# Optimization experiments

Hardware: AMD Instinct MI355X
Metric: run time of the kernel (lower is better)

## Reference

```python
import jax, jax.numpy as jnp
import numpy as np


def _pairwise_sq(x, y):
    # squared euclidean distances [B,N,M] via gram trick (avoids [B,N,M,D] temp)
    x2 = jnp.sum(x * x, -1)[:, :, None]
    y2 = jnp.sum(y * y, -1)[:, None, :]
    return x2 + y2 - 2.0 * jnp.einsum('bnd,bmd->bnm', x, y)


def _dtw_dp(C):
    # Subsequence DTW accumulated-cost matrix. C: [N,M].
    # D[0,:] = C[0,:] (free start anywhere in y);
    # D[i,j] = C[i,j] + min(D[i-1,j], D[i-1,j-1], D[i,j-1]).
    # Within-row recurrence D[i,j] = min(a[j], D[i,j-1] + C[i,j]) with
    # a[j] = min(D[i-1,j], D[i-1,j-1]) + C[i,j] is a min-plus prefix scan:
    # D[i,j] = S[j] + cummin(a - S)[j], S = cumsum(C[i]).
    inf = jnp.asarray(jnp.inf, C.dtype)
    def row(Dprev, Crow):
        shifted = jnp.concatenate([jnp.full((1,), inf, C.dtype), Dprev[:-1]])
        a = jnp.minimum(Dprev, shifted) + Crow
        S = jnp.cumsum(Crow)
        D = S + jax.lax.cummin(a - S)
        return D, D
    _, Dr = jax.lax.scan(row, C[0], C[1:])
    return jnp.concatenate([C[0][None], Dr], 0)


def _backtrack(D):
    # Backtrack optimal subseq-DTW path from (N-1, argmin D[-1]) to row 0.
    # Returns, per x index i, the largest y index aligned to i on the path
    # (== last occurrence kept by dict(dtw_path) in the torch code).
    N, M = D.shape
    inf = jnp.asarray(jnp.inf, D.dtype)
    j0 = jnp.argmin(D[-1]).astype(jnp.int32)
    i0 = jnp.asarray(N - 1, jnp.int32)
    yl = jnp.zeros((N,), jnp.int32).at[i0].set(j0)
    def step(carry, _):
        i, j, yl = carry
        dd = jnp.where(j > 0, D[i - 1, j - 1], inf)
        du = D[i - 1, j]
        dl = jnp.where(j > 0, D[i, j - 1], inf)
        best = jnp.minimum(jnp.minimum(dd, du), dl)
        take_d = dd == best
        take_u = (~take_d) & (du == best)
        ni = jnp.where(take_d | take_u, i - 1, i)
        nj = jnp.where(take_d, j - 1, jnp.where(take_u, j, j - 1))
        active = i > 0
        ni = jnp.where(active, ni, i)
        nj = jnp.where(active, nj, j)
        yl = jnp.where(active, yl.at[ni].max(nj), yl)
        return (ni, nj, yl), None
    (_, _, yl), _ = jax.lax.scan(step, (i0, j0, yl), None, length=N + M)
    return yl


def setup_inputs() -> dict:
    key = jax.random.key(0)
    k0, k1, k2, k3 = jax.random.split(key, 4)
    B, N, M, D = 16, 1024, 4096, 64
    return {
        'x': jax.random.normal(k0, (B, N, D), jnp.float32),
        'y': jax.random.normal(k1, (B, M, D), jnp.float32),
        'x_t': jax.random.uniform(k2, (B, N), dtype=jnp.float32),
        'y_t': jax.random.uniform(k3, (B, M), dtype=jnp.float32),
    }


def reference(x, y, x_t, y_t):
    C = _pairwise_sq(x, y)                      # [B,N,M]
    D = jax.vmap(_dtw_dp)(C)                    # [B,N,M]
    # total path cost == DP optimum (sum of C along the optimal path)
    dtw_cost = jnp.min(D[:, -1, :], axis=-1)    # [B]
    y_last = jax.vmap(_backtrack)(jax.lax.stop_gradient(D))  # [B,N] int32
    w_ts = x_t                                  # path covers all x indices 0..N-1 in order
    w_vs = jnp.take_along_axis(y_t, y_last, axis=1)
    return dtw_cost, w_ts, w_vs
```

## Files before the change

### kernel.cpp

```cpp
#include <hip/hip_runtime.h>

#define B_ 16
#define N_ 1024
#define M_ 4096
#define D_ 64
#define SROWS_ (N_ + 63)
#define SROWSP_ (SROWS_ + 17)
#define SPAIR_ 544
#define TSB_ ((size_t)SPAIR_ * 128)
#define BTQ_ 96
#define BTROWS_ 128
#define GEMM_BLKS_ 2048

__device__ __forceinline__ float finf() { return __builtin_inff(); }

__device__ __forceinline__ float wave_shr1(float x) {
  return __int_as_float(__builtin_amdgcn_update_dpp(
      0, __float_as_int(x), 0x138, 0xF, 0xF, false));
}
__device__ __forceinline__ float rdlane(float v, int l) {
  return __int_as_float(__builtin_amdgcn_readlane(__float_as_int(v), l));
}

__global__ void prep_kernel(const float* __restrict__ x,
                            const float* __restrict__ x_t,
                            float* __restrict__ x2,
                            float* __restrict__ w_ts_out) {
  int id = blockIdx.x * blockDim.x + threadIdx.x;
  const float4* xr = (const float4*)(x + (size_t)id * D_);
  float s = 0.f;
#pragma unroll
  for (int e = 0; e < D_ / 4; ++e) {
    float4 v = xr[e];
    s += v.x * v.x + v.y * v.y + v.z * v.z + v.w * v.w;
  }
  x2[id] = s;
  w_ts_out[id] = x_t[id];
}

__device__ __forceinline__ void gemm_body(
    const float* __restrict__ x, const float* __restrict__ y,
    const float* __restrict__ x2, float* __restrict__ Cs, int chunkBase,
    int b, int tile, int ibeg, int t, char* smem) {
  float4* ylds = (float4*)smem;
  float4* xlds = (float4*)(smem + 65536);
  float* y2lds = (float*)(smem + 73728);
  const int cg = t & 63;
  const int rg = t >> 6;
  float* CsT = Cs + (size_t)(b * 4 + tile) * SROWSP_ * 256;

  {
    const int j = chunkBase + tile * 256 + t;
    const float4* yrow = (const float4*)(y + ((size_t)b * M_ + j) * D_);
    float4 yr[16];
#pragma unroll
    for (int e = 0; e < 16; ++e) yr[e] = yrow[e];
    float y2 = 0.f;
#pragma unroll
    for (int e = 0; e < 16; ++e)
      y2 += yr[e].x * yr[e].x + yr[e].y * yr[e].y + yr[e].z * yr[e].z +
            yr[e].w * yr[e].w;
    y2lds[t] = y2;
#pragma unroll
    for (int e = 0; e < 16; ++e) ylds[e * 256 + t] = yr[e];
  }
  if (t < 128) {
    const int row = t >> 2;
    const int part = t & 3;
    const float4* xr = (const float4*)(x + ((size_t)b * N_ + ibeg + row) * D_);
#pragma unroll
    for (int k = 0; k < 4; ++k) {
      const int e = part * 4 + k;
      xlds[e * 32 + row] = xr[e];
    }
  }
  __syncthreads();

  const int r0 = rg * 8;
  float acc[8][4];
#pragma unroll
  for (int r = 0; r < 8; ++r)
#pragma unroll
    for (int c = 0; c < 4; ++c) acc[r][c] = 0.f;

#pragma unroll
  for (int kb = 0; kb < 4; ++kb) {
    float4 yf[4][4];
#pragma unroll
    for (int c = 0; c < 4; ++c)
#pragma unroll
      for (int ee = 0; ee < 4; ++ee)
        yf[c][ee] = ylds[(kb * 4 + ee) * 256 + cg + 64 * c];
#pragma unroll
    for (int r = 0; r < 8; ++r) {
      float4 xv[4];
#pragma unroll
      for (int ee = 0; ee < 4; ++ee)
        xv[ee] = xlds[(kb * 4 + ee) * 32 + r0 + r];
#pragma unroll
      for (int ee = 0; ee < 4; ++ee) {
#pragma unroll
        for (int c = 0; c < 4; ++c) {
          acc[r][c] += xv[ee].x * yf[c][ee].x + xv[ee].y * yf[c][ee].y +
                       xv[ee].z * yf[c][ee].z + xv[ee].w * yf[c][ee].w;
        }
      }
    }
  }

#pragma unroll
  for (int r = 0; r < 8; ++r) {
    const int i = ibeg + r0 + r;
    const float xx = x2[b * N_ + i];
#pragma unroll
    for (int c = 0; c < 4; ++c) {
      const int ct = cg + 64 * c;
      const int l = ct >> 2;
      CsT[(size_t)(i + l) * 256 + ct] = xx + y2lds[ct] - 2.f * acc[r][c];
    }
  }
}

__global__ __launch_bounds__(256) void gemm_kernel(
    const float* __restrict__ x, const float* __restrict__ y,
    const float* __restrict__ x2, float* __restrict__ Cs, int chunkBase) {
  __shared__ __align__(16) char smem[74752];
  gemm_body(x, y, x2, Cs, chunkBase, blockIdx.z, blockIdx.x, blockIdx.y * 32,
            threadIdx.x, smem);
}

__global__ __launch_bounds__(256) void dtw_fused(
    const float* __restrict__ x, const float* __restrict__ y,
    const float* __restrict__ x2, const float* __restrict__ CsRead,
    float* __restrict__ CsWrite, int nextBase,
    unsigned char* __restrict__ dec, const float* __restrict__ carryIn,
    float* __restrict__ carryOut, float* __restrict__ partV,
    int* __restrict__ partJ, int chunk, int hasCarry) {
  __shared__ __align__(16) char smem[90112];
  const int bid = blockIdx.x;
  const int t = threadIdx.x;

  if (bid >= B_) {
    const int gb = bid - B_;
    gemm_body(x, y, x2, CsWrite, nextBase, gb >> 7, gb & 3,
              ((gb >> 2) & 31) * 32, t, smem);
    return;
  }

  float(*ring)[1024] = reinterpret_cast<float(*)[1024]>(smem);
  float* cring = reinterpret_cast<float*>(smem + 12288);
  int* prog = reinterpret_cast<int*>(smem + 16384);
  float* redV = reinterpret_cast<float*>(smem + 16400);
  int* redJ = reinterpret_cast<int*>(smem + 16416);
  volatile int* vProg = prog;

  const int b = bid;
  const int lane = t & 63;
  const int W = t >> 6;

  if (t < 3) prog[t] = -1;
  const float* cIn = carryIn + b * N_;
  if (hasCarry) ((float4*)cring)[t] = ((const float4*)cIn)[t];
  __syncthreads();

  const float INF = finf();
  const float* loadP = CsRead + (size_t)(b * 4 + W) * SROWSP_ * 256;
  const int tileG = chunk * 4 + W;
  unsigned short* decP =
      (unsigned short*)(dec + (size_t)(b * 16 + tileG) * TSB_) + lane;
  float* carryB = carryOut + b * N_;
  const int jbase = tileG * 256 + lane * 4;

  float4 cc0 = ((const float4*)(loadP + 0 * 256))[lane];
  float4 cc1 = ((const float4*)(loadP + 1 * 256))[lane];
  float4 cc2 = ((const float4*)(loadP + 2 * 256))[lane];
  float4 cc3 = ((const float4*)(loadP + 3 * 256))[lane];
  float4 cc4 = ((const float4*)(loadP + 4 * 256))[lane];
  float4 cc5 = ((const float4*)(loadP + 5 * 256))[lane];
  float4 cc6 = ((const float4*)(loadP + 6 * 256))[lane];
  float4 cc7 = ((const float4*)(loadP + 7 * 256))[lane];
  loadP += 8 * 256;

  float edgeVec = INF, lvPrev = INF;
  float up0 = 0.f, up1 = 0.f, up2 = 0.f, up3 = 0.f;
  float dpp1 = INF, dpp2 = INF;
  float fin0 = INF, fin1 = INF, fin2 = INF, fin3 = INF;
  float ebuf[8];

#define BLOCKHEAD()                                                           \
  {                                                                           \
    if (W > 0) {                                                              \
      if (sb < N_) {                                                          \
        const int tgt = sb + 7;                                               \
        while (vProg[W - 1] < tgt) {}                                         \
        asm volatile("" ::: "memory");                                        \
        lvPrev = rdlane(edgeVec, 7);                                          \
        edgeVec = ring[W - 1][(sb + lane) & 1023];                            \
      }                                                                       \
    } else if (hasCarry) {                                                    \
      lvPrev = rdlane(edgeVec, 7);                                            \
      if (sb < N_) edgeVec = cring[(sb + lane) & 1023];                       \
    }                                                                         \
  }

#define DPSTEP(KK, CCV, ROW0, FIN)                                            \
  {                                                                           \
    const float lv = rdlane(edgeVec, (KK));                                   \
    const float left = (lane == 0) ? lv : dpp1;                               \
    const float diag = (lane == 0) ? lvPrev : dpp2;                           \
    lvPrev = lv;                                                              \
    float bv0 = fminf(diag, fminf(up0, left));                                \
    unsigned int pk = (diag <= bv0) ? 0u : ((up0 <= bv0) ? 1u : 2u);          \
    if (ROW0) bv0 = (sb + (KK) == lane) ? 0.f : bv0;                          \
    const float D0 = CCV.x + bv0;                                             \
    float bv1 = fminf(up0, fminf(up1, D0));                                   \
    pk |= (up0 <= bv1) ? 0u : ((up1 <= bv1) ? 4u : 8u);                       \
    if (ROW0) bv1 = (sb + (KK) == lane) ? 0.f : bv1;                          \
    const float D1 = CCV.y + bv1;                                             \
    float bv2 = fminf(up1, fminf(up2, D1));                                   \
    pk |= (up1 <= bv2) ? 0u : ((up2 <= bv2) ? 16u : 32u);                     \
    if (ROW0) bv2 = (sb + (KK) == lane) ? 0.f : bv2;                          \
    const float D2 = CCV.z + bv2;                                             \
    float bv3 = fminf(up2, fminf(up3, D2));                                   \
    pk |= (up2 <= bv3) ? 0u : ((up3 <= bv3) ? 64u : 128u);                    \
    if (ROW0) bv3 = (sb + (KK) == lane) ? 0.f : bv3;                          \
    const float D3 = CCV.w + bv3;                                             \
    ebuf[(KK)] = D3;                                                          \
    if ((KK) & 1) {                                                           \
      pk16 |= pk << 8;                                                        \
      decP[((KK) >> 1) * 64] = (unsigned short)pk16;                          \
    } else {                                                                  \
      pk16 = pk;                                                              \
    }                                                                         \
    if (FIN) {                                                                \
      const bool lr = (sb + (KK) == 1023 + lane);                             \
      fin0 = lr ? D0 : fin0; fin1 = lr ? D1 : fin1;                           \
      fin2 = lr ? D2 : fin2; fin3 = lr ? D3 : fin3;                           \
    }                                                                         \
    const float sh = wave_shr1(D3);                                           \
    dpp2 = dpp1; dpp1 = sh;                                                   \
    up0 = D0; up1 = D1; up2 = D2; up3 = D3;                                   \
    CCV = ((const float4*)(loadP + (KK) * 256))[lane];                        \
  }

#define BLOCKEND()                                                            \
  {                                                                           \
    const int r0 = sb - 63;                                                   \
    if (W < 3) {                                                              \
      if (lane == 63 && r0 > -8 && r0 < N_) {                                 \
        _Pragma("unroll") for (int k = 0; k < 8; ++k) {                       \
          const int r = r0 + k;                                               \
          if ((unsigned)r < (unsigned)N_) ring[W][r] = ebuf[k];               \
        }                                                                     \
        __builtin_amdgcn_s_waitcnt(0xC07F);                                   \
        vProg[W] = r0 + 7;                                                    \
      }                                                                       \
    } else if (chunk < 3) {                                                   \
      if (lane == 63 && r0 > -8 && r0 < N_) {                                 \
        _Pragma("unroll") for (int k = 0; k < 8; ++k) {                       \
          const int r = r0 + k;                                               \
          if ((unsigned)r < (unsigned)N_) carryB[r] = ebuf[k];                \
        }                                                                     \
      }                                                                       \
    }                                                                         \
    loadP += 8 * 256;                                                         \
    decP += 256;                                                              \
  }

#define STEP8(R0, FN)                                                         \
  DPSTEP(0, cc0, R0, FN) DPSTEP(1, cc1, R0, FN) DPSTEP(2, cc2, R0, FN)        \
  DPSTEP(3, cc3, R0, FN) DPSTEP(4, cc4, R0, FN) DPSTEP(5, cc5, R0, FN)        \
  DPSTEP(6, cc6, R0, FN) DPSTEP(7, cc7, R0, FN)

  int sb = 0;
  for (; sb < 64; sb += 8) {
    BLOCKHEAD();
    unsigned int pk16;
    STEP8(1, 0)
    BLOCKEND();
  }
  for (; sb < 1016; sb += 8) {
    BLOCKHEAD();
    unsigned int pk16;
    STEP8(0, 0)
    BLOCKEND();
  }
  for (; sb < 1088; sb += 8) {
    BLOCKHEAD();
    unsigned int pk16;
    STEP8(0, 1)
    BLOCKEND();
  }
#undef DPSTEP
#undef STEP8
#undef BLOCKHEAD
#undef BLOCKEND

  float mv = fin0; int mj = jbase;
  if (fin1 < mv) { mv = fin1; mj = jbase + 1; }
  if (fin2 < mv) { mv = fin2; mj = jbase + 2; }
  if (fin3 < mv) { mv = fin3; mj = jbase + 3; }
#pragma unroll
  for (int off = 32; off > 0; off >>= 1) {
    const float ov = __shfl_down(mv, off);
    const int oj = __shfl_down(mj, off);
    if (ov < mv || (ov == mv && oj < mj)) { mv = ov; mj = oj; }
  }
  if (lane == 0) { redV[W] = mv; redJ[W] = mj; }
  __syncthreads();
  if (t == 0) {
    float bm = redV[0]; int bj = redJ[0];
#pragma unroll
    for (int w = 1; w < 4; ++w)
      if (redV[w] < bm) { bm = redV[w]; bj = redJ[w]; }
    partV[b * 4 + chunk] = bm;
    partJ[b * 4 + chunk] = bj;
  }
}

__global__ __launch_bounds__(64) void backtrack_kernel(
    const unsigned char* __restrict__ dec, const float* __restrict__ partV,
    const int* __restrict__ partJ, int nch, const float* __restrict__ y_t,
    float* __restrict__ w_vs, float* __restrict__ cost_out) {
  const int b = blockIdx.x;
  const int lane = threadIdx.x;
  __shared__ unsigned int stage[3 * 3072];
  __shared__ unsigned short tab[BTROWS_][BTQ_ * 4 + 2];
  __shared__ int st_i, st_j;
  __shared__ int jrow[BTROWS_ + 1];
  const unsigned char* db = dec + (size_t)b * 16 * TSB_;
  const float* yt = y_t + b * M_;
  float* wv = w_vs + b * N_;

  if (lane == 0) {
    float bc = finf(); int bj = 0;
    for (int c = 0; c < nch; ++c) {
      const float v = partV[b * nch + c];
      const int j = partJ[b * nch + c];
      if (v < bc) { bc = v; bj = j; }
    }
    cost_out[b] = bc;
    st_i = N_ - 1;
    st_j = bj;
    wv[N_ - 1] = yt[bj];
  }
  for (;;) {
    __syncthreads();
    const int i = st_i, j = st_j;
    if (i <= 0) break;
    const int qj = j >> 2;
    int qlo = qj - (BTQ_ - 1);
    if (qlo < 0) qlo = 0;
    const int Tbase = qlo >> 6;
    int plo = (i - 127) >> 1;
    if (plo < 0) plo = 0;

#pragma unroll
    for (int tt = 0; tt < 3; ++tt) {
      int T = Tbase + tt;
      if (T > 15) T = 15;
      const uint4* src =
          (const uint4*)(db + (size_t)T * TSB_ + (size_t)plo * 128);
#pragma unroll
      for (int v = 0; v < 12; ++v) {
        const int wb = tt * 12288 + (v * 64 + lane) * 16;
        const int sw = wb ^ (((wb >> 7) & 7) << 4);
        *(uint4*)((char*)stage + sw) = src[v * 64 + lane];
      }
    }
    __syncthreads();

    const unsigned char* sb8 = (const unsigned char*)stage;
#pragma unroll
    for (int half = 0; half < 2; ++half) {
      const int r = i - lane - half * 64;
      if (r >= 1) {
        unsigned char wr[BTQ_];
#pragma unroll
        for (int k = 0; k < BTQ_; ++k) {
          const int q = qlo + k;
          const int tt = (q >> 6) - Tbase;
          const int l = q & 63;
          const int s = r + l;
          int idx = tt * 12288 + ((s >> 1) - plo) * 128 + l * 2 + (s & 1);
          idx ^= ((idx >> 7) & 7) << 4;
          wr[k] = sb8[idx];
        }
        unsigned short run = 0xFFFF;
        const int tr = lane + half * 64;
#pragma unroll
        for (int k = 0; k < BTQ_; ++k) {
          const unsigned int byte = wr[k];
#pragma unroll
          for (int cs = 0; cs < 4; ++cs) {
            const unsigned int code = (byte >> (2 * cs)) & 3u;
            const int c = 4 * k + cs;
            const unsigned short v =
                (code != 2u) ? (unsigned short)((c << 2) | code) : run;
            tab[tr][c] = v;
            run = v;
          }
        }
      }
    }
    __syncthreads();
    if (lane == 0) {
      const int base = qlo << 2;
      int rr = i, cj = j;
      while (rr >= 1 && (i - rr) < BTROWS_) {
        const int l = i - rr;
        const int c = cj - base;
        if (c < 0) break;
        const unsigned short v = tab[l][c];
        if (v == 0xFFFF) { cj = base - 1; break; }
        const int e = v >> 2;
        const int ce = v & 3;
        cj = base + e - (ce == 0 ? 1 : 0);
        --rr;
        jrow[i - rr] = cj;
      }
      st_i = rr;
      st_j = cj;
    }
    __syncthreads();
    const int cnt = i - st_i;
    if (lane < cnt) wv[i - 1 - lane] = yt[jrow[lane + 1]];
    {
      const int l2 = lane + 64;
      if (l2 < cnt) wv[i - 1 - l2] = yt[jrow[l2 + 1]];
    }
  }
}

extern "C" void kernel_launch(void* const* d_in, const int* in_sizes, int n_in,
                              void* d_out, int out_size, void* d_ws, size_t ws_size,
                              hipStream_t stream) {
  const float* x = (const float*)d_in[0];
  const float* y = (const float*)d_in[1];
  const float* x_t = (const float*)d_in[2];
  const float* y_t = (const float*)d_in[3];

  float* out_cost = (float*)d_out;
  float* out_wts = out_cost + B_;
  float* out_wvs = out_wts + B_ * N_;

  const size_t csBytes = (size_t)B_ * 4 * SROWSP_ * 256 * 4;
  const size_t decBytes = (size_t)B_ * 16 * TSB_;
  const size_t x2Bytes = (size_t)B_ * N_ * 4;
  const size_t tailBytes = x2Bytes + 2 * (size_t)B_ * N_ * 4 + B_ * 4 * 8;

  const int overlap = ws_size >= 2 * csBytes + decBytes + tailBytes;
  const int nCs = overlap ? 2 : 1;

  char* ws = (char*)d_ws;
  float* CsA = (float*)ws;
  float* CsB = overlap ? (float*)(ws + csBytes) : CsA;
  unsigned char* dec = (unsigned char*)(ws + (size_t)nCs * csBytes);
  float* x2 = (float*)(ws + (size_t)nCs * csBytes + decBytes);
  float* carryA = x2 + B_ * N_;
  float* carryB = carryA + B_ * N_;
  float* partV = carryB + B_ * N_;
  int* partJ = (int*)(partV + B_ * 4);

  prep_kernel<<<dim3((B_ * N_) / 256), 256, 0, stream>>>(x, x_t, x2, out_wts);

  float* cbuf[2] = {carryA, carryB};
  if (overlap) {
    gemm_kernel<<<dim3(4, N_ / 32, B_), 256, 0, stream>>>(x, y, x2, CsA, 0);
    for (int c = 0; c < 4; ++c) {
      float* csR = (c & 1) ? CsB : CsA;
      float* csW = (c & 1) ? CsA : CsB;
      const int nblk = B_ + (c < 3 ? GEMM_BLKS_ : 0);
      dtw_fused<<<dim3(nblk), 256, 0, stream>>>(
          x, y, x2, csR, csW, (c + 1) * 1024, dec, cbuf[(c + 1) & 1],
          cbuf[c & 1], partV, partJ, c, c > 0 ? 1 : 0);
    }
  } else {
    for (int c = 0; c < 4; ++c) {
      gemm_kernel<<<dim3(4, N_ / 32, B_), 256, 0, stream>>>(x, y, x2, CsA,
                                                            c * 1024);
      dtw_fused<<<dim3(B_), 256, 0, stream>>>(
          x, y, x2, CsA, CsA, 0, dec, cbuf[(c + 1) & 1], cbuf[c & 1], partV,
          partJ, c, c > 0 ? 1 : 0);
    }
  }

  backtrack_kernel<<<dim3(B_), 64, 0, stream>>>(dec, partV, partJ, 4, y_t,
                                                out_wvs, out_cost);
}
```

Measured before the change: 1.012 ms.

## Pipeline DTW column chunks across concurrent blocks with global progress flags

Adds a single persistent dtw_pipe kernel in which each batch gets four DP blocks, one per 1024-column chunk. Each block waits on a GEMM completion counter and then on a per-row carry progress flag published through global memory, so the chunks run as a wavefront instead of as four serialized launches. The GEMM blocks for later chunks run inside the same launch, and the full cost matrix is stored when workspace allows. This removes the inter-launch serialization and the one-block-per-batch DP bottleneck. In exchange it relies on spin-waiting across blocks, which can deadlock if the dependent blocks are not co-resident, and it needs a much larger workspace.

```diff
diff --git a/kernel.cpp b/kernel.cpp
--- a/kernel.cpp
+++ b/kernel.cpp
@@ -25,8 +25,11 @@
 __global__ void prep_kernel(const float* __restrict__ x,
                             const float* __restrict__ x_t,
                             float* __restrict__ x2,
-                            float* __restrict__ w_ts_out) {
+                            float* __restrict__ w_ts_out,
+                            int* __restrict__ ctrl) {
   int id = blockIdx.x * blockDim.x + threadIdx.x;
+  if (ctrl && blockIdx.x == 0 && threadIdx.x < 128)
+    ctrl[threadIdx.x] = (threadIdx.x < 64) ? 0 : -1;
   const float4* xr = (const float4*)(x + (size_t)id * D_);
   float s = 0.f;
 #pragma unroll
@@ -40,17 +43,16 @@
 
 __device__ __forceinline__ void gemm_body(
     const float* __restrict__ x, const float* __restrict__ y,
-    const float* __restrict__ x2, float* __restrict__ Cs, int chunkBase,
-    int b, int tile, int ibeg, int t, char* smem) {
+    const float* __restrict__ x2, float* __restrict__ CsT, int jcol0,
+    int b, int ibeg, int t, char* smem) {
   float4* ylds = (float4*)smem;
   float4* xlds = (float4*)(smem + 65536);
   float* y2lds = (float*)(smem + 73728);
+
   const int cg = t & 63;
   const int rg = t >> 6;
-  float* CsT = Cs + (size_t)(b * 4 + tile) * SROWSP_ * 256;
-
   {
-    const int j = chunkBase + tile * 256 + t;
+    const int j = jcol0 + t;
     const float4* yrow = (const float4*)(y + ((size_t)b * M_ + j) * D_);
     float4 yr[16];
 #pragma unroll
@@ -123,10 +125,241 @@
 
 __global__ __launch_bounds__(256) void gemm_kernel(
     const float* __restrict__ x, const float* __restrict__ y,
-    const float* __restrict__ x2, float* __restrict__ Cs, int chunkBase) {
+    const float* __restrict__ x2, float* __restrict__ Cs, int chunkBase,
+    int nt, int tileOff) {
   __shared__ __align__(16) char smem[74752];
-  gemm_body(x, y, x2, Cs, chunkBase, blockIdx.z, blockIdx.x, blockIdx.y * 32,
+  const int tile = blockIdx.x;
+  const int b = blockIdx.z;
+  float* CsT =
+      Cs + ((size_t)b * nt + tileOff + tile) * SROWSP_ * 256;
+  gemm_body(x, y, x2, CsT, chunkBase + tile * 256, b, blockIdx.y * 32,
             threadIdx.x, smem);
+}
+
+__global__ __launch_bounds__(256) void dtw_pipe(
+    const float* __restrict__ x, const float* __restrict__ y,
+    const float* __restrict__ x2, float* __restrict__ Cs,
+    unsigned char* __restrict__ dec, float* __restrict__ carryPipe,
+    int* __restrict__ gemmCnt, int* __restrict__ carryProg,
+    float* __restrict__ partV, int* __restrict__ partJ) {
+  __shared__ __align__(16) char smem[90112];
+  const int bid = blockIdx.x;
+  const int t = threadIdx.x;
+
+  if (bid >= 64) {
+    const int gb = bid - 64;
+    const int chunk = 1 + (gb >> 11);
+    const int g2 = gb & 2047;
+    const int b = g2 >> 7;
+    const int tile = g2 & 3;
+    const int ibeg = ((g2 >> 2) & 31) * 32;
+    float* CsT =
+        Cs + ((size_t)b * 16 + chunk * 4 + tile) * SROWSP_ * 256;
+    gemm_body(x, y, x2, CsT, chunk * 1024 + tile * 256, b, ibeg, t, smem);
+    __syncthreads();
+    if (t == 0) {
+      __threadfence();
+      atomicAdd(&gemmCnt[b * 4 + chunk], 1);
+    }
+    return;
+  }
+
+  const int b = bid >> 2;
+  const int C = bid & 3;
+  const int lane = t & 63;
+  const int W = t >> 6;
+
+  float(*ring)[1024] = reinterpret_cast<float(*)[1024]>(smem);
+  int* prog = reinterpret_cast<int*>(smem + 12288);
+  float* redV = reinterpret_cast<float*>(smem + 12352);
+  int* redJ = reinterpret_cast<int*>(smem + 12384);
+  volatile int* vProg = prog;
+
+  if (t < 3) prog[t] = -1;
+
+  if (C > 0) {
+    if (t == 0) {
+      while (__hip_atomic_load(&gemmCnt[b * 4 + C], __ATOMIC_ACQUIRE,
+                               __HIP_MEMORY_SCOPE_AGENT) < 128)
+        __builtin_amdgcn_s_sleep(8);
+      __threadfence();
+    }
+    __syncthreads();
+  } else {
+    __syncthreads();
+  }
+
+  const float INF = finf();
+  const float* loadP = Cs + ((size_t)b * 16 + C * 4 + W) * SROWSP_ * 256;
+  const int tileG = C * 4 + W;
+  unsigned short* decP =
+      (unsigned short*)(dec + (size_t)(b * 16 + tileG) * TSB_) + lane;
+  const float* carryIn = carryPipe + ((size_t)b * 3 + (C > 0 ? C - 1 : 0)) * N_;
+  float* carryOut = carryPipe + ((size_t)b * 3 + (C < 3 ? C : 0)) * N_;
+  int* progIn = &carryProg[b * 4 + (C > 0 ? C - 1 : 0)];
+  int* progOut = &carryProg[b * 4 + C];
+  const int jbase = tileG * 256 + lane * 4;
+
+  float4 cc0 = ((const float4*)(loadP + 0 * 256))[lane];
+  float4 cc1 = ((const float4*)(loadP + 1 * 256))[lane];
+  float4 cc2 = ((const float4*)(loadP + 2 * 256))[lane];
+  float4 cc3 = ((const float4*)(loadP + 3 * 256))[lane];
+  float4 cc4 = ((const float4*)(loadP + 4 * 256))[lane];
+  float4 cc5 = ((const float4*)(loadP + 5 * 256))[lane];
+  float4 cc6 = ((const float4*)(loadP + 6 * 256))[lane];
+  float4 cc7 = ((const float4*)(loadP + 7 * 256))[lane];
+  loadP += 8 * 256;
+
+  float edgeVec = INF, lvPrev = INF;
+  float up0 = 0.f, up1 = 0.f, up2 = 0.f, up3 = 0.f;
+  float dpp1 = INF, dpp2 = INF;
+  float fin0 = INF, fin1 = INF, fin2 = INF, fin3 = INF;
+  float ebuf[8];
+
+#define BLOCKHEADP()                                                          \
+  {                                                                           \
+    if (W > 0) {                                                              \
+      if (sb < N_) {                                                          \
+        const int tgt = sb + 7;                                               \
+        while (vProg[W - 1] < tgt) {}                                         \
+        asm volatile("" ::: "memory");                                        \
+        lvPrev = rdlane(edgeVec, 7);                                          \
+        edgeVec = ring[W - 1][(sb + lane) & 1023];                            \
+      }                                                                       \
+    } else if (C > 0) {                                                       \
+      if (((sb & 63) == 0) && sb < N_) {                                      \
+        const int tgt = sb + 63;                                              \
+        if (lane == 0) {                                                      \
+          while (__hip_atomic_load(progIn, __ATOMIC_ACQUIRE,                  \
+                                   __HIP_MEMORY_SCOPE_AGENT) < tgt)           \
+            __builtin_amdgcn_s_sleep(4);                                      \
+        }                                                                     \
+        edgeVec = carryIn[(sb + lane) & 1023];                                \
+      }                                                                       \
+    }                                                                         \
+  }
+
+#define DPSTEP(KK, CCV, ROW0, FIN)                                            \
+  {                                                                           \
+    const float lv = rdlane(edgeVec, eb + (KK));                              \
+    const float left = (lane == 0) ? lv : dpp1;                               \
+    const float diag = (lane == 0) ? lvPrev : dpp2;                           \
+    lvPrev = lv;                                                              \
+    float bv0 = fminf(diag, fminf(up0, left));                                \
+    unsigned int pk = (diag <= bv0) ? 0u : ((up0 <= bv0) ? 1u : 2u);          \
+    if (ROW0) bv0 = (sb + (KK) == lane) ? 0.f : bv0;                          \
+    const float D0 = CCV.x + bv0;                                             \
+    float bv1 = fminf(up0, fminf(up1, D0));                                   \
+    pk |= (up0 <= bv1) ? 0u : ((up1 <= bv1) ? 4u : 8u);                       \
+    if (ROW0) bv1 = (sb + (KK) == lane) ? 0.f : bv1;                          \
+    const float D1 = CCV.y + bv1;                                             \
+    float bv2 = fminf(up1, fminf(up2, D1));                                   \
+    pk |= (up1 <= bv2) ? 0u : ((up2 <= bv2) ? 16u : 32u);                     \
+    if (ROW0) bv2 = (sb + (KK) == lane) ? 0.f : bv2;                          \
+    const float D2 = CCV.z + bv2;                                             \
+    float bv3 = fminf(up2, fminf(up3, D2));                                   \
+    pk |= (up2 <= bv3) ? 0u : ((up3 <= bv3) ? 64u : 128u);                    \
+    if (ROW0) bv3 = (sb + (KK) == lane) ? 0.f : bv3;                          \
+    const float D3 = CCV.w + bv3;                                             \
+    ebuf[(KK)] = D3;                                                          \
+    if ((KK) & 1) {                                                           \
+      pk16 |= pk << 8;                                                        \
+      decP[((KK) >> 1) * 64] = (unsigned short)pk16;                          \
+    } else {                                                                  \
+      pk16 = pk;                                                              \
+    }                                                                         \
+    if (FIN) {                                                                \
+      const bool lr = (sb + (KK) == 1023 + lane);                             \
+      fin0 = lr ? D0 : fin0; fin1 = lr ? D1 : fin1;                           \
+      fin2 = lr ? D2 : fin2; fin3 = lr ? D3 : fin3;                           \
+    }                                                                         \
+    const float sh = wave_shr1(D3);                                           \
+    dpp2 = dpp1; dpp1 = sh;                                                   \
+    up0 = D0; up1 = D1; up2 = D2; up3 = D3;                                   \
+    CCV = ((const float4*)(loadP + (KK) * 256))[lane];                        \
+  }
+
+#define BLOCKENDP()                                                           \
+  {                                                                           \
+    const int r0 = sb - 63;                                                   \
+    if (W < 3) {                                                              \
+      if (lane == 63 && r0 > -8 && r0 < N_) {                                 \
+        _Pragma("unroll") for (int k = 0; k < 8; ++k) {                       \
+          const int r = r0 + k;                                               \
+          if ((unsigned)r < (unsigned)N_) ring[W][r] = ebuf[k];               \
+        }                                                                     \
+        __builtin_amdgcn_s_waitcnt(0xC07F);                                   \
+        vProg[W] = r0 + 7;                                                    \
+      }                                                                       \
+    } else if (C < 3) {                                                       \
+      if (lane == 63) {                                                       \
+        if (r0 > -8 && r0 < N_) {                                             \
+          _Pragma("unroll") for (int k = 0; k < 8; ++k) {                     \
+            const int r = r0 + k;                                             \
+            if ((unsigned)r < (unsigned)N_) carryOut[r] = ebuf[k];            \
+          }                                                                   \
+        }                                                                     \
+        if ((sb & 63) == 56)                                                  \
+          __hip_atomic_store(progOut, sb - 56, __ATOMIC_RELEASE,              \
+                             __HIP_MEMORY_SCOPE_AGENT);                       \
+      }                                                                       \
+    }                                                                         \
+    loadP += 8 * 256;                                                         \
+    decP += 256;                                                              \
+  }
+
+#define STEP8(R0, FN)                                                         \
+  DPSTEP(0, cc0, R0, FN) DPSTEP(1, cc1, R0, FN) DPSTEP(2, cc2, R0, FN)        \
+  DPSTEP(3, cc3, R0, FN) DPSTEP(4, cc4, R0, FN) DPSTEP(5, cc5, R0, FN)        \
+  DPSTEP(6, cc6, R0, FN) DPSTEP(7, cc7, R0, FN)
+
+  int sb = 0;
+  for (; sb < 64; sb += 8) {
+    BLOCKHEADP();
+    const int eb = (W == 0) ? (sb & 56) : 0;
+    unsigned int pk16;
+    STEP8(1, 0)
+    BLOCKENDP();
+  }
+  for (; sb < 1016; sb += 8) {
+    BLOCKHEADP();
+    const int eb = (W == 0) ? (sb & 56) : 0;
+    unsigned int pk16;
+    STEP8(0, 0)
+    BLOCKENDP();
+  }
+  for (; sb < 1088; sb += 8) {
+    BLOCKHEADP();
+    const int eb = (W == 0) ? (sb & 56) : 0;
+    unsigned int pk16;
+    STEP8(0, 1)
+    BLOCKENDP();
+  }
+#undef DPSTEP
+#undef STEP8
+#undef BLOCKHEADP
+#undef BLOCKENDP
+
+  float mv = fin0; int mj = jbase;
+  if (fin1 < mv) { mv = fin1; mj = jbase + 1; }
+  if (fin2 < mv) { mv = fin2; mj = jbase + 2; }
+  if (fin3 < mv) { mv = fin3; mj = jbase + 3; }
+#pragma unroll
+  for (int off = 32; off > 0; off >>= 1) {
+    const float ov = __shfl_down(mv, off);
+    const int oj = __shfl_down(mj, off);
+    if (ov < mv || (ov == mv && oj < mj)) { mv = ov; mj = oj; }
+  }
+  if (lane == 0) { redV[W] = mv; redJ[W] = mj; }
+  __syncthreads();
+  if (t == 0) {
+    float bm = redV[0]; int bj = redJ[0];
+#pragma unroll
+    for (int w = 1; w < 4; ++w)
+      if (redV[w] < bm) { bm = redV[w]; bj = redJ[w]; }
+    partV[b * 4 + C] = bm;
+    partJ[b * 4 + C] = bj;
+  }
 }
 
 __global__ __launch_bounds__(256) void dtw_fused(
@@ -142,8 +375,11 @@
 
   if (bid >= B_) {
     const int gb = bid - B_;
-    gemm_body(x, y, x2, CsWrite, nextBase, gb >> 7, gb & 3,
-              ((gb >> 2) & 31) * 32, t, smem);
+    const int b = gb >> 7;
+    const int tile = gb & 3;
+    const int ibeg = ((gb >> 2) & 31) * 32;
+    float* CsT = CsWrite + ((size_t)b * 4 + tile) * SROWSP_ * 256;
+    gemm_body(x, y, x2, CsT, nextBase + tile * 256, b, ibeg, t, smem);
     return;
   }
 
@@ -444,29 +680,53 @@
   float* out_wts = out_cost + B_;
   float* out_wvs = out_wts + B_ * N_;
 
-  const size_t csBytes = (size_t)B_ * 4 * SROWSP_ * 256 * 4;
+  const size_t csChunk = (size_t)B_ * 4 * SROWSP_ * 256 * 4;
+  const size_t csFull = (size_t)B_ * 16 * SROWSP_ * 256 * 4;
   const size_t decBytes = (size_t)B_ * 16 * TSB_;
   const size_t x2Bytes = (size_t)B_ * N_ * 4;
-  const size_t tailBytes = x2Bytes + 2 * (size_t)B_ * N_ * 4 + B_ * 4 * 8;
-
-  const int overlap = ws_size >= 2 * csBytes + decBytes + tailBytes;
+  const size_t pipeTail = x2Bytes + 3 * (size_t)B_ * N_ * 4 + 4096;
+  const size_t r6Tail = x2Bytes + 2 * (size_t)B_ * N_ * 4 + B_ * 4 * 8;
+
+  char* ws = (char*)d_ws;
+
+  if (ws_size >= csFull + decBytes + pipeTail) {
+    float* Cs = (float*)ws;
+    unsigned char* dec = (unsigned char*)(ws + csFull);
+    float* x2 = (float*)(ws + csFull + decBytes);
+    float* carryPipe = x2 + B_ * N_;
+    float* partV = carryPipe + 3 * B_ * N_;
+    int* partJ = (int*)(partV + 64);
+    int* ctrl = partJ + 64;
+
+    prep_kernel<<<dim3((B_ * N_) / 256), 256, 0, stream>>>(x, x_t, x2,
+                                                           out_wts, ctrl);
+    gemm_kernel<<<dim3(4, N_ / 32, B_), 256, 0, stream>>>(x, y, x2, Cs, 0,
+                                                          16, 0);
+    dtw_pipe<<<dim3(64 + 3 * GEMM_BLKS_), 256, 0, stream>>>(
+        x, y, x2, Cs, dec, carryPipe, ctrl, ctrl + 64, partV, partJ);
+    backtrack_kernel<<<dim3(B_), 64, 0, stream>>>(dec, partV, partJ, 4, y_t,
+                                                  out_wvs, out_cost);
+    return;
+  }
+
+  const int overlap = ws_size >= 2 * csChunk + decBytes + r6Tail;
   const int nCs = overlap ? 2 : 1;
-
-  char* ws = (char*)d_ws;
   float* CsA = (float*)ws;
-  float* CsB = overlap ? (float*)(ws + csBytes) : CsA;
-  unsigned char* dec = (unsigned char*)(ws + (size_t)nCs * csBytes);
-  float* x2 = (float*)(ws + (size_t)nCs * csBytes + decBytes);
+  float* CsB = overlap ? (float*)(ws + csChunk) : CsA;
+  unsigned char* dec = (unsigned char*)(ws + (size_t)nCs * csChunk);
+  float* x2 = (float*)(ws + (size_t)nCs * csChunk + decBytes);
   float* carryA = x2 + B_ * N_;
   float* carryB = carryA + B_ * N_;
   float* partV = carryB + B_ * N_;
   int* partJ = (int*)(partV + B_ * 4);
 
-  prep_kernel<<<dim3((B_ * N_) / 256), 256, 0, stream>>>(x, x_t, x2, out_wts);
+  prep_kernel<<<dim3((B_ * N_) / 256), 256, 0, stream>>>(x, x_t, x2, out_wts,
+                                                         nullptr);
 
   float* cbuf[2] = {carryA, carryB};
   if (overlap) {
-    gemm_kernel<<<dim3(4, N_ / 32, B_), 256, 0, stream>>>(x, y, x2, CsA, 0);
+    gemm_kernel<<<dim3(4, N_ / 32, B_), 256, 0, stream>>>(x, y, x2, CsA, 0,
+                                                          4, 0);
     for (int c = 0; c < 4; ++c) {
       float* csR = (c & 1) ? CsB : CsA;
       float* csW = (c & 1) ? CsA : CsB;
@@ -478,7 +738,7 @@
   } else {
     for (int c = 0; c < 4; ++c) {
       gemm_kernel<<<dim3(4, N_ / 32, B_), 256, 0, stream>>>(x, y, x2, CsA,
-                                                            c * 1024);
+                                                            c * 1024, 4, 0);
       dtw_fused<<<dim3(B_), 256, 0, stream>>>(
           x, y, x2, CsA, CsA, 0, dec, cbuf[(c + 1) & 1], cbuf[c & 1], partV,
           partJ, c, c > 0 ? 1 : 0);
```

New measurement: 1.009 ms. No clear change (-0.3%).
